# Kernel optimization log

Hardware: AMD Instinct MI355X
Metric: run time of the kernel (lower is better)

## Reference

```python
import jax, jax.numpy as jnp
import numpy as np

B, T, HID = 2, 2048, 2048
NH = 8
D = HID // NH  # head_dim = 256 (expand_ratio=1 so input_dim == hidden_size)
EPS_RMS = 1e-8   # RMSNorm inside BitLinear
EPS_LN = 1e-5    # layernorm_eps for g_norm


def _rms(x, w, eps):
    # weighted RMSNorm over last dim
    return x * jax.lax.rsqrt(jnp.mean(x * x, axis=-1, keepdims=True) + eps) * w


def _act_quant(x):
    # per-token 8-bit fake quant with straight-through estimator
    s = 127.0 / jnp.clip(jnp.max(jnp.abs(x), axis=-1, keepdims=True), 1e-5)
    q = jnp.clip(jnp.round(x * s), -128, 127) / s
    return x + jax.lax.stop_gradient(q - x)


def _weight_quant(w):
    # ternary weight quantization (BitNet b1.58) with STE
    s = 1.0 / jnp.clip(jnp.mean(jnp.abs(w)), 1e-5)
    q = jnp.clip(jnp.round(w * s), -1, 1) / s
    return w + jax.lax.stop_gradient(q - w)


def _bitlinear(x, w, norm_w):
    # FusedBitLinear: RMSNorm -> activation quant -> ternary-weight linear
    xq = _act_quant(_rms(x, norm_w, EPS_RMS))
    return jnp.einsum('btk,ok->bto', xq, _weight_quant(w))


def setup_inputs() -> dict:
    key = jax.random.key(0)
    ks = jax.random.split(key, 5)
    std = 2 ** (-2.5) * np.sqrt(2.0 / (HID + HID))  # xavier_uniform-ish std with gain 2^-2.5
    return {
        'hidden_states': jax.random.normal(ks[0], (B, T, HID), dtype=jnp.float32),
        'w_i': jax.random.normal(ks[1], (HID, HID), dtype=jnp.float32) * std,
        'w_f': jax.random.normal(ks[2], (HID, HID), dtype=jnp.float32) * std,
        'w_g': jax.random.normal(ks[3], (HID, HID), dtype=jnp.float32) * std,
        'w_o': jax.random.normal(ks[4], (HID, HID), dtype=jnp.float32) * std,
        'n_i': jnp.ones((HID,), jnp.float32),
        'n_f': jnp.ones((HID,), jnp.float32),
        'n_g': jnp.ones((HID,), jnp.float32),
        'n_o': jnp.ones((HID,), jnp.float32),
        'gn_w': jnp.ones((HID,), jnp.float32),
    }


def reference(hidden_states, w_i, w_f, w_g, w_o, n_i, n_f, n_g, n_o, gn_w):
    hs = hidden_states
    i = _bitlinear(hs, w_i, n_i)                      # [B,T,HID]
    f = jax.nn.sigmoid(_bitlinear(hs, w_f, n_f))      # forget gate
    # swiglu(i, 1 - f) = silu(i) * (1 - f)
    i = i * jax.nn.sigmoid(i) * (1.0 - f)

    # b l (h d) -> t b h d for scan
    def to_tbhd(x):
        return x.reshape(B, T, NH, D).transpose(1, 0, 2, 3)

    i_t, f_t = to_tbhd(i), to_tbhd(f)

    def step(h, ft_it):
        ft, it = ft_it
        h = ft * h + it
        return h, h

    h0 = jnp.zeros((B, NH, D), dtype=i.dtype)
    _, o = jax.lax.scan(step, h0, (f_t, i_t))         # [T,B,NH,D]
    o = o.transpose(1, 0, 2, 3).reshape(B, T, HID)     # b l (h d)

    # g_norm(g_proj(hs), o): rmsnorm(g) * o * sigmoid(o)
    g = _bitlinear(hs, w_g, n_g)
    o = _rms(g, gn_w, EPS_LN) * o * jax.nn.sigmoid(o)
    return _bitlinear(o, w_o, n_o)
```

## Files before the change

### kernel.cpp

```cpp
#include <hip/hip_runtime.h>
#include <math.h>

#define HID 2048
#define TOKENS 4096
#define TT 2048
#define NCH 4096
#define NC 32
#define CL 64
#define WELEM 4194304

typedef unsigned short u16;
typedef signed char i8;
typedef int i32x4 __attribute__((ext_vector_type(4)));

__device__ inline float sigm(float x) { return 1.0f / (1.0f + expf(-x)); }
__device__ inline u16 f2bf_rn(float v) {
  unsigned b = __float_as_uint(v);
  unsigned r = b + 0x7FFFu + ((b >> 16) & 1u);
  return (u16)(r >> 16);
}
__device__ inline float bf2f(u16 h) {
  return __uint_as_float((unsigned)h << 16);
}

__device__ inline float wred_sum(float v) {
#pragma unroll
  for (int o = 32; o > 0; o >>= 1) v += __shfl_down(v, o);
  return v;
}
__device__ inline float wred_max(float v) {
#pragma unroll
  for (int o = 32; o > 0; o >>= 1) v = fmaxf(v, __shfl_down(v, o));
  return v;
}
__device__ inline double wred_sumd(double v) {
#pragma unroll
  for (int o = 32; o > 0; o >>= 1) v += __shfl_down(v, o);
  return v;
}

__device__ __forceinline__ void gl_lds16(const void* g, void* l) {
  __builtin_amdgcn_global_load_lds(
      (__attribute__((address_space(1))) void*)(void*)g,
      (__attribute__((address_space(3))) void*)l, 16, 0, 0);
}

__device__ __forceinline__ int pack8(const int* qi) {
  return (qi[0] & 255) | ((qi[1] & 255) << 8) | ((qi[2] & 255) << 16)
       | ((qi[3] & 255) << 24);
}

__global__ __launch_bounds__(256) void absmean_kernel(
    const float* __restrict__ w0, const float* __restrict__ w1,
    const float* __restrict__ w2, const float* __restrict__ w3,
    double* __restrict__ wsum) {
  int widx = blockIdx.x >> 9;
  int blk = blockIdx.x & 511;
  const float* w = widx == 0 ? w0 : widx == 1 ? w1 : widx == 2 ? w2 : w3;
  size_t base = (size_t)blk * 8192;
  double acc = 0.0;
#pragma unroll
  for (int r = 0; r < 8; ++r) {
    float4 v = *(const float4*)&w[base + (size_t)(r * 256 + threadIdx.x) * 4];
    acc += (double)fabsf(v.x) + (double)fabsf(v.y) + (double)fabsf(v.z) +
           (double)fabsf(v.w);
  }
  acc = wred_sumd(acc);
  __shared__ double sh[4];
  int tid = threadIdx.x;
  if ((tid & 63) == 0) sh[tid >> 6] = acc;
  __syncthreads();
  if (tid == 0) atomicAdd(&wsum[widx], (sh[0] + sh[1]) + (sh[2] + sh[3]));
}

__global__ __launch_bounds__(256) void wquant4_kernel(
    const float* __restrict__ w0, const float* __restrict__ w1,
    const float* __restrict__ w2, const float* __restrict__ w3,
    const double* __restrict__ wsum, i8* __restrict__ q0, i8* __restrict__ q1,
    i8* __restrict__ q2, i8* __restrict__ q3) {
  int sel = blockIdx.x >> 11;
  int blk = blockIdx.x & 2047;
  const float* w = sel == 0 ? w0 : sel == 1 ? w1 : sel == 2 ? w2 : w3;
  i8* wq = sel == 0 ? q0 : sel == 1 ? q1 : sel == 2 ? q2 : q3;
  int widx = sel == 0 ? 1 : sel == 1 ? 0 : sel;
  double mean = wsum[widx] * (1.0 / (double)WELEM);
  float s = (float)(1.0 / fmax(mean, 1e-5));
  size_t base = (size_t)blk * 2048 + (size_t)threadIdx.x * 8;
  float4 va = *(const float4*)&w[base];
  float4 vb = *(const float4*)&w[base + 4];
  float vv[8] = {va.x, va.y, va.z, va.w, vb.x, vb.y, vb.z, vb.w};
  int qi[8];
#pragma unroll
  for (int j = 0; j < 8; ++j) {
    float q1v = rintf(vv[j] * s);
    q1v = fminf(fmaxf(q1v, -1.0f), 1.0f);
    qi[j] = (int)q1v;
  }
  *(int2*)&wq[base] = make_int2(pack8(qi), pack8(qi + 4));
}

__global__ __launch_bounds__(256) void rmsquant3_kernel(
    const float* __restrict__ X, const float* __restrict__ nw0,
    const float* __restrict__ nw1, const float* __restrict__ nw2,
    i8* __restrict__ Xq0, i8* __restrict__ Xq1, i8* __restrict__ Xq2,
    float* __restrict__ inv0, float* __restrict__ inv1,
    float* __restrict__ inv2) {
  int tok = blockIdx.x;
  int tid = threadIdx.x;
  const float* xrow = X + (size_t)tok * HID;
  int c0 = tid * 8;
  float x[8];
  *(float4*)&x[0] = *(const float4*)&xrow[c0];
  *(float4*)&x[4] = *(const float4*)&xrow[c0 + 4];
  float ss = 0.0f;
#pragma unroll
  for (int j = 0; j < 8; ++j) ss += x[j] * x[j];
  __shared__ float sh[4];
  float v = wred_sum(ss);
  if ((tid & 63) == 0) sh[tid >> 6] = v;
  __syncthreads();
  float tot = (sh[0] + sh[1]) + (sh[2] + sh[3]);
  float rstd = (float)(1.0 / sqrt((double)(tot * (1.0f / HID)) + 1e-8));
#pragma unroll
  for (int pass = 0; pass < 3; ++pass) {
    const float* nw = pass == 0 ? nw0 : pass == 1 ? nw1 : nw2;
    i8* Xq = pass == 0 ? Xq0 : pass == 1 ? Xq1 : Xq2;
    float* inv_s = pass == 0 ? inv0 : pass == 1 ? inv1 : inv2;
    float y[8];
    float amax = 0.0f;
#pragma unroll
    for (int j = 0; j < 8; ++j) {
      y[j] = x[j] * rstd * nw[c0 + j];
      amax = fmaxf(amax, fabsf(y[j]));
    }
    __syncthreads();
    float vv = wred_max(amax);
    if ((tid & 63) == 0) sh[tid >> 6] = vv;
    __syncthreads();
    float am = fmaxf(fmaxf(fmaxf(sh[0], sh[1]), fmaxf(sh[2], sh[3])), 1e-5f);
    float s = 127.0f / am;
    int qi[8];
#pragma unroll
    for (int j = 0; j < 8; ++j) {
      float qq = rintf(y[j] * s);
      qq = fminf(fmaxf(qq, -128.0f), 127.0f);
      qi[j] = (int)qq;
    }
    *(int2*)&Xq[(size_t)tok * HID + c0] = make_int2(pack8(qi), pack8(qi + 4));
    if (tid == 0) inv_s[tok] = am * (1.0f / 127.0f);
  }
}

template <int NSEG, bool F32OUT>
__global__ __launch_bounds__(512) void gemm8_kernel(
    const i8* __restrict__ A0, const i8* __restrict__ A1,
    const i8* __restrict__ A2, const i8* __restrict__ W0,
    const i8* __restrict__ W1, const i8* __restrict__ W2,
    const float* __restrict__ inv0, const float* __restrict__ inv1,
    const float* __restrict__ inv2, const double* __restrict__ wsum,
    int widx0, int widx1, int widx2, void* __restrict__ O0,
    void* __restrict__ O1, void* __restrict__ O2) {
  const int tid = threadIdx.x;
  const int cpx = gridDim.x >> 3;
  const int lid = blockIdx.x;
  const int swz = (lid & 7) * cpx + (lid >> 3);
  const int seg = NSEG == 1 ? 0 : (swz >> 9);
  const int idx = swz & 511;
  const int n0 = (idx & 15) * 128;
  const int m0 = (idx >> 4) * 128;

  const i8* Aq = seg == 0 ? A0 : seg == 1 ? A1 : A2;
  const i8* Wq = seg == 0 ? W0 : seg == 1 ? W1 : W2;
  const float* inv_s = seg == 0 ? inv0 : seg == 1 ? inv1 : inv2;
  void* Out = seg == 0 ? O0 : seg == 1 ? O1 : O2;
  const int widx = seg == 0 ? widx0 : seg == 1 ? widx1 : widx2;

  __shared__ __align__(16) i8 As[2][16384];
  __shared__ __align__(16) i8 Bs[2][16384];
  float wscale = (float)fmax(wsum[widx] * (1.0 / (double)WELEM), 1e-5);

  const int wave = tid >> 6, lane = tid & 63;
  const int wm = wave >> 2;
  const int wn = wave & 3;
  const int lrow = lane & 15;
  const int ksel = lane >> 4;
  const int rsw = lrow & 7;
  const int srow8 = lane >> 3;
  const int scol = ((lane & 7) ^ srow8) << 4;

  const i8* Ab = Aq + (size_t)m0 * HID;
  const i8* Wb = Wq + (size_t)n0 * HID;

  i32x4 acc[4][2];
#pragma unroll
  for (int i = 0; i < 4; ++i)
#pragma unroll
    for (int j = 0; j < 2; ++j)
#pragma unroll
      for (int r = 0; r < 4; ++r) acc[i][j][r] = 0;

#define STAGE(buf, k0)                                                      \
  {                                                                         \
    _Pragma("unroll") for (int c = 0; c < 2; ++c) {                         \
      int chunk = wave * 2 + c;                                             \
      int row = chunk * 8 + srow8;                                          \
      gl_lds16(&Ab[(size_t)row * HID + (k0) + scol], &As[buf][chunk * 1024]); \
      gl_lds16(&Wb[(size_t)row * HID + (k0) + scol], &Bs[buf][chunk * 1024]); \
    }                                                                       \
  }

  const int NT = HID / 128;
  STAGE(0, 0)
  __syncthreads();
  int cur = 0;
  for (int kt = 0; kt < NT; ++kt) {
    if (kt + 1 < NT) STAGE(cur ^ 1, (kt + 1) * 128)
    i32x4 af[4][2], bfr[2][2];
#pragma unroll
    for (int i = 0; i < 4; ++i) {
      int ra = wm * 64 + i * 16 + lrow;
#pragma unroll
      for (int kk = 0; kk < 2; ++kk) {
        int phys = ((kk << 2) | ksel) ^ rsw;
        af[i][kk] = *(const i32x4*)&As[cur][ra * 128 + phys * 16];
      }
    }
#pragma unroll
    for (int j = 0; j < 2; ++j) {
      int rb = wn * 32 + j * 16 + lrow;
#pragma unroll
      for (int kk = 0; kk < 2; ++kk) {
        int phys = ((kk << 2) | ksel) ^ rsw;
        bfr[j][kk] = *(const i32x4*)&Bs[cur][rb * 128 + phys * 16];
      }
    }
    __builtin_amdgcn_s_setprio(1);
#pragma unroll
    for (int kk = 0; kk < 2; ++kk)
#pragma unroll
      for (int i = 0; i < 4; ++i)
#pragma unroll
        for (int j = 0; j < 2; ++j)
          acc[i][j] = __builtin_amdgcn_mfma_i32_16x16x64_i8(
              af[i][kk], bfr[j][kk], acc[i][j], 0, 0, 0);
    __builtin_amdgcn_s_setprio(0);
    __syncthreads();
    cur ^= 1;
  }
#undef STAGE

#pragma unroll
  for (int i = 0; i < 4; ++i) {
    int rbase = m0 + wm * 64 + i * 16 + (lane >> 4) * 4;
#pragma unroll
    for (int j = 0; j < 2; ++j) {
      int col = n0 + wn * 32 + j * 16 + lrow;
#pragma unroll
      for (int r = 0; r < 4; ++r) {
        int row = rbase + r;
        float v = (float)acc[i][j][r] * inv_s[row] * wscale;
        float rr;
        if (NSEG == 3)
          rr = seg == 0 ? sigm(v) : seg == 1 ? v * sigm(v) : v;
        else
          rr = v;
        size_t oidx = (size_t)row * HID + col;
        if (F32OUT)
          ((float*)Out)[oidx] = rr;
        else
          ((u16*)Out)[oidx] = f2bf_rn(rr);
      }
    }
  }
}

__global__ __launch_bounds__(256) void scan1_kernel(
    const u16* __restrict__ F, u16* __restrict__ IO, float* __restrict__ P,
    float* __restrict__ H) {
  int c = blockIdx.x * 256 + threadIdx.x;
  int q = blockIdx.y;
  size_t base =
      (size_t)(c >> 11) * TT * HID + (c & 2047) + (size_t)q * CL * HID;
  float h = 0.0f, p = 1.0f;
#pragma unroll 4
  for (int t = 0; t < CL; ++t) {
    size_t idx = base + (size_t)t * HID;
    float f = bf2f(F[idx]);
    float iv = bf2f(IO[idx]);
    h = fmaf(f, h, iv - iv * f);
    p *= f;
    IO[idx] = f2bf_rn(h);
  }
  P[q * NCH + c] = p;
  H[q * NCH + c] = h;
}

__global__ __launch_bounds__(256) void scan2_kernel(
    const float* __restrict__ P, const float* __restrict__ H,
    float* __restrict__ Ini) {
  int c = blockIdx.x * 256 + threadIdx.x;
  float carry = 0.0f;
#pragma unroll
  for (int q = 0; q < NC; ++q) {
    float pq = P[q * NCH + c];
    float hq = H[q * NCH + c];
    Ini[q * NCH + c] = carry;
    carry = fmaf(pq, carry, hq);
  }
}

__global__ __launch_bounds__(256) void scan3_kernel(
    const u16* __restrict__ F, const float* __restrict__ Ini,
    u16* __restrict__ IO) {
  int c = blockIdx.x * 256 + threadIdx.x;
  int q = blockIdx.y + 1;
  float h0 = Ini[q * NCH + c];
  if (h0 == 0.0f) return;
  size_t base =
      (size_t)(c >> 11) * TT * HID + (c & 2047) + (size_t)q * CL * HID;
  float p = 1.0f;
#pragma unroll 4
  for (int t = 0; t < CL; ++t) {
    size_t idx = base + (size_t)t * HID;
    p *= bf2f(F[idx]);
    IO[idx] = f2bf_rn(fmaf(p, h0, bf2f(IO[idx])));
  }
}

__global__ __launch_bounds__(256) void combine_quant_kernel(
    const u16* __restrict__ G, const float* __restrict__ gnw,
    const u16* __restrict__ O, const float* __restrict__ nw,
    i8* __restrict__ Xq, float* __restrict__ inv_s) {
  int tok = blockIdx.x;
  int tid = threadIdx.x;
  int c0 = tid * 8;
  const u16* grow = G + (size_t)tok * HID;
  const u16* orow = O + (size_t)tok * HID;
  ushort4 ga = *(const ushort4*)&grow[c0];
  ushort4 gb = *(const ushort4*)&grow[c0 + 4];
  ushort4 oa = *(const ushort4*)&orow[c0];
  ushort4 ob = *(const ushort4*)&orow[c0 + 4];
  float g[8] = {bf2f(ga.x), bf2f(ga.y), bf2f(ga.z), bf2f(ga.w),
                bf2f(gb.x), bf2f(gb.y), bf2f(gb.z), bf2f(gb.w)};
  float o[8] = {bf2f(oa.x), bf2f(oa.y), bf2f(oa.z), bf2f(oa.w),
                bf2f(ob.x), bf2f(ob.y), bf2f(ob.z), bf2f(ob.w)};
  __shared__ float sh[4];
  float ss = 0.0f;
#pragma unroll
  for (int j = 0; j < 8; ++j) ss += g[j] * g[j];
  float v = wred_sum(ss);
  if ((tid & 63) == 0) sh[tid >> 6] = v;
  __syncthreads();
  float tot = (sh[0] + sh[1]) + (sh[2] + sh[3]);
  float rstd_g = (float)(1.0 / sqrt((double)(tot * (1.0f / HID)) + 1e-5));
  float on[8];
  float ss2 = 0.0f;
#pragma unroll
  for (int j = 0; j < 8; ++j) {
    on[j] = g[j] * rstd_g * gnw[c0 + j] * o[j] * sigm(o[j]);
    ss2 += on[j] * on[j];
  }
  __syncthreads();
  v = wred_sum(ss2);
  if ((tid & 63) == 0) sh[tid >> 6] = v;
  __syncthreads();
  float tot2 = (sh[0] + sh[1]) + (sh[2] + sh[3]);
  float rstd_o = (float)(1.0 / sqrt((double)(tot2 * (1.0f / HID)) + 1e-8));
  float y[8];
  float amax = 0.0f;
#pragma unroll
  for (int j = 0; j < 8; ++j) {
    y[j] = on[j] * rstd_o * nw[c0 + j];
    amax = fmaxf(amax, fabsf(y[j]));
  }
  __syncthreads();
  v = wred_max(amax);
  if ((tid & 63) == 0) sh[tid >> 6] = v;
  __syncthreads();
  float am = fmaxf(fmaxf(fmaxf(sh[0], sh[1]), fmaxf(sh[2], sh[3])), 1e-5f);
  float s = 127.0f / am;
  int qi[8];
#pragma unroll
  for (int j = 0; j < 8; ++j) {
    float qq = rintf(y[j] * s);
    qq = fminf(fmaxf(qq, -128.0f), 127.0f);
    qi[j] = (int)qq;
  }
  *(int2*)&Xq[(size_t)tok * HID + c0] = make_int2(pack8(qi), pack8(qi + 4));
  if (tid == 0) inv_s[tok] = am * (1.0f / 127.0f);
}

extern "C" void kernel_launch(void* const* d_in, const int* in_sizes, int n_in,
                              void* d_out, int out_size, void* d_ws,
                              size_t ws_size, hipStream_t stream) {
  const float* hs = (const float*)d_in[0];
  const float* w_i = (const float*)d_in[1];
  const float* w_f = (const float*)d_in[2];
  const float* w_g = (const float*)d_in[3];
  const float* w_o = (const float*)d_in[4];
  const float* n_i = (const float*)d_in[5];
  const float* n_f = (const float*)d_in[6];
  const float* n_g = (const float*)d_in[7];
  const float* n_o = (const float*)d_in[8];
  const float* gn_w = (const float*)d_in[9];
  float* Out = (float*)d_out;

  char* ws = (char*)d_ws;
  i8* WQ0 = (i8*)ws;
  i8* WQ1 = (i8*)(ws + 4194304);
  i8* WQ2 = (i8*)(ws + 8388608);
  i8* WQ3 = (i8*)(ws + 12582912);
  i8* XQ0 = (i8*)(ws + 16777216);
  i8* XQ1 = (i8*)(ws + 25165824);
  i8* XQ2 = (i8*)(ws + 33554432);
  u16* F = (u16*)(ws + 41943040);
  u16* OB = (u16*)(ws + 58720256);
  u16* G = (u16*)(ws + 75497472);
  float* invs0 = (float*)(ws + 92274688);
  float* invs1 = (float*)(ws + 92291072);
  float* invs2 = (float*)(ws + 92307456);
  double* wsum = (double*)(ws + 92323840);
  float* scanP = (float*)(ws + 92324864);
  float* scanH = (float*)(ws + 92849152);

  hipMemsetAsync(wsum, 0, 4 * sizeof(double), stream);
  absmean_kernel<<<2048, 256, 0, stream>>>(w_i, w_f, w_g, w_o, wsum);

  wquant4_kernel<<<8192, 256, 0, stream>>>(w_f, w_i, w_g, w_o, wsum, WQ0, WQ1,
                                           WQ2, WQ3);
  rmsquant3_kernel<<<TOKENS, 256, 0, stream>>>(hs, n_f, n_i, n_g, XQ0, XQ1,
                                               XQ2, invs0, invs1, invs2);

  gemm8_kernel<3, false><<<1536, 512, 0, stream>>>(
      XQ0, XQ1, XQ2, WQ0, WQ1, WQ2, invs0, invs1, invs2, wsum, 1, 0, 2, F, OB,
      G);

  scan1_kernel<<<dim3(NCH / 256, NC), 256, 0, stream>>>(F, OB, scanP, scanH);
  scan2_kernel<<<NCH / 256, 256, 0, stream>>>(scanP, scanH, scanP);
  scan3_kernel<<<dim3(NCH / 256, NC - 1), 256, 0, stream>>>(F, scanP, OB);

  combine_quant_kernel<<<TOKENS, 256, 0, stream>>>(G, gn_w, OB, n_o, XQ0,
                                                   invs0);

  gemm8_kernel<1, true><<<512, 512, 0, stream>>>(
      XQ0, XQ0, XQ0, WQ3, WQ3, WQ3, invs0, invs0, invs0, wsum, 3, 3, 3, Out,
      Out, Out);
}
```

Baseline: 200.9 us.

## Enlarge GEMM tile to 128x256 with BK=64, fuse prep and scan kernels

The int8 GEMM tile grows from 128x128 to 128x256 with a K step of 64 and a new LDS swizzle. This doubles the accumulators per wave and halves the grid, to cut global and LDS traffic per MFMA. The weight-quant and activation-quant kernels are merged into one launch, and scan2/scan3 are fused so each block recomputes its chunk carry serially, trading launches for redundant work. The larger tile raises register pressure and leaves fewer blocks (768 and 256) on the device, which may underfill the CUs.

New measurement: 217.6 us. 1.08x slower.

```diff
diff --git a/kernel.cpp b/kernel.cpp
--- a/kernel.cpp
+++ b/kernel.cpp
@@ -73,39 +73,38 @@
   if (tid == 0) atomicAdd(&wsum[widx], (sh[0] + sh[1]) + (sh[2] + sh[3]));
 }
 
-__global__ __launch_bounds__(256) void wquant4_kernel(
+__global__ __launch_bounds__(256) void prep_kernel(
     const float* __restrict__ w0, const float* __restrict__ w1,
     const float* __restrict__ w2, const float* __restrict__ w3,
     const double* __restrict__ wsum, i8* __restrict__ q0, i8* __restrict__ q1,
-    i8* __restrict__ q2, i8* __restrict__ q3) {
-  int sel = blockIdx.x >> 11;
-  int blk = blockIdx.x & 2047;
-  const float* w = sel == 0 ? w0 : sel == 1 ? w1 : sel == 2 ? w2 : w3;
-  i8* wq = sel == 0 ? q0 : sel == 1 ? q1 : sel == 2 ? q2 : q3;
-  int widx = sel == 0 ? 1 : sel == 1 ? 0 : sel;
-  double mean = wsum[widx] * (1.0 / (double)WELEM);
-  float s = (float)(1.0 / fmax(mean, 1e-5));
-  size_t base = (size_t)blk * 2048 + (size_t)threadIdx.x * 8;
-  float4 va = *(const float4*)&w[base];
-  float4 vb = *(const float4*)&w[base + 4];
-  float vv[8] = {va.x, va.y, va.z, va.w, vb.x, vb.y, vb.z, vb.w};
-  int qi[8];
-#pragma unroll
-  for (int j = 0; j < 8; ++j) {
-    float q1v = rintf(vv[j] * s);
-    q1v = fminf(fmaxf(q1v, -1.0f), 1.0f);
-    qi[j] = (int)q1v;
-  }
-  *(int2*)&wq[base] = make_int2(pack8(qi), pack8(qi + 4));
-}
-
-__global__ __launch_bounds__(256) void rmsquant3_kernel(
-    const float* __restrict__ X, const float* __restrict__ nw0,
-    const float* __restrict__ nw1, const float* __restrict__ nw2,
-    i8* __restrict__ Xq0, i8* __restrict__ Xq1, i8* __restrict__ Xq2,
-    float* __restrict__ inv0, float* __restrict__ inv1,
+    i8* __restrict__ q2, i8* __restrict__ q3, const float* __restrict__ X,
+    const float* __restrict__ nw0, const float* __restrict__ nw1,
+    const float* __restrict__ nw2, i8* __restrict__ Xq0, i8* __restrict__ Xq1,
+    i8* __restrict__ Xq2, float* __restrict__ inv0, float* __restrict__ inv1,
     float* __restrict__ inv2) {
-  int tok = blockIdx.x;
+  if (blockIdx.x < 8192) {
+    int sel = blockIdx.x >> 11;
+    int blk = blockIdx.x & 2047;
+    const float* w = sel == 0 ? w0 : sel == 1 ? w1 : sel == 2 ? w2 : w3;
+    i8* wq = sel == 0 ? q0 : sel == 1 ? q1 : sel == 2 ? q2 : q3;
+    int widx = sel == 0 ? 1 : sel == 1 ? 0 : sel;
+    double mean = wsum[widx] * (1.0 / (double)WELEM);
+    float s = (float)(1.0 / fmax(mean, 1e-5));
+    size_t base = (size_t)blk * 2048 + (size_t)threadIdx.x * 8;
+    float4 va = *(const float4*)&w[base];
+    float4 vb = *(const float4*)&w[base + 4];
+    float vv[8] = {va.x, va.y, va.z, va.w, vb.x, vb.y, vb.z, vb.w};
+    int qi[8];
+#pragma unroll
+    for (int j = 0; j < 8; ++j) {
+      float q1v = rintf(vv[j] * s);
+      q1v = fminf(fmaxf(q1v, -1.0f), 1.0f);
+      qi[j] = (int)q1v;
+    }
+    *(int2*)&wq[base] = make_int2(pack8(qi), pack8(qi + 4));
+    return;
+  }
+  int tok = blockIdx.x - 8192;
   int tid = threadIdx.x;
   const float* xrow = X + (size_t)tok * HID;
   int c0 = tid * 8;
@@ -152,7 +151,7 @@
 }
 
 template <int NSEG, bool F32OUT>
-__global__ __launch_bounds__(512) void gemm8_kernel(
+__global__ __launch_bounds__(512, 4) void gemm8_kernel(
     const i8* __restrict__ A0, const i8* __restrict__ A1,
     const i8* __restrict__ A2, const i8* __restrict__ W0,
     const i8* __restrict__ W1, const i8* __restrict__ W2,
@@ -164,10 +163,10 @@
   const int cpx = gridDim.x >> 3;
   const int lid = blockIdx.x;
   const int swz = (lid & 7) * cpx + (lid >> 3);
-  const int seg = NSEG == 1 ? 0 : (swz >> 9);
-  const int idx = swz & 511;
-  const int n0 = (idx & 15) * 128;
-  const int m0 = (idx >> 4) * 128;
+  const int seg = NSEG == 1 ? 0 : (swz >> 8);
+  const int idx = swz & 255;
+  const int n0 = (idx & 7) * 256;
+  const int m0 = (idx >> 3) * 128;
 
   const i8* Aq = seg == 0 ? A0 : seg == 1 ? A1 : A2;
   const i8* Wq = seg == 0 ? W0 : seg == 1 ? W1 : W2;
@@ -175,7 +174,7 @@
   void* Out = seg == 0 ? O0 : seg == 1 ? O1 : O2;
   const int widx = seg == 0 ? widx0 : seg == 1 ? widx1 : widx2;
 
-  __shared__ __align__(16) i8 As[2][16384];
+  __shared__ __align__(16) i8 As[2][8192];
   __shared__ __align__(16) i8 Bs[2][16384];
   float wscale = (float)fmax(wsum[widx] * (1.0 / (double)WELEM), 1e-5);
 
@@ -184,65 +183,57 @@
   const int wn = wave & 3;
   const int lrow = lane & 15;
   const int ksel = lane >> 4;
-  const int rsw = lrow & 7;
-  const int srow8 = lane >> 3;
-  const int scol = ((lane & 7) ^ srow8) << 4;
+  const int phys = ((ksel ^ ((lrow >> 1) & 3)) << 4);
+  const int srl = lane >> 2;
+  const int sg = (lane >> 3) & 3;
+  const int skoff = ((lane & 3) ^ sg) << 4;
 
   const i8* Ab = Aq + (size_t)m0 * HID;
   const i8* Wb = Wq + (size_t)n0 * HID;
 
-  i32x4 acc[4][2];
+  i32x4 acc[4][4];
 #pragma unroll
   for (int i = 0; i < 4; ++i)
 #pragma unroll
-    for (int j = 0; j < 2; ++j)
+    for (int j = 0; j < 4; ++j)
 #pragma unroll
       for (int r = 0; r < 4; ++r) acc[i][j][r] = 0;
 
-#define STAGE(buf, k0)                                                      \
-  {                                                                         \
-    _Pragma("unroll") for (int c = 0; c < 2; ++c) {                         \
-      int chunk = wave * 2 + c;                                             \
-      int row = chunk * 8 + srow8;                                          \
-      gl_lds16(&Ab[(size_t)row * HID + (k0) + scol], &As[buf][chunk * 1024]); \
-      gl_lds16(&Wb[(size_t)row * HID + (k0) + scol], &Bs[buf][chunk * 1024]); \
-    }                                                                       \
-  }
-
-  const int NT = HID / 128;
+#define STAGE(buf, k0)                                                        \
+  {                                                                           \
+    int rowA = wave * 16 + srl;                                               \
+    gl_lds16(&Ab[(size_t)rowA * HID + (k0) + skoff], &As[buf][wave * 1024]);  \
+    int rowB0 = wave * 32 + srl;                                              \
+    gl_lds16(&Wb[(size_t)rowB0 * HID + (k0) + skoff], &Bs[buf][wave * 2048]); \
+    int rowB1 = wave * 32 + 16 + srl;                                         \
+    gl_lds16(&Wb[(size_t)rowB1 * HID + (k0) + skoff],                         \
+             &Bs[buf][wave * 2048 + 1024]);                                   \
+  }
+
+  const int NT = HID / 64;
   STAGE(0, 0)
   __syncthreads();
   int cur = 0;
   for (int kt = 0; kt < NT; ++kt) {
-    if (kt + 1 < NT) STAGE(cur ^ 1, (kt + 1) * 128)
-    i32x4 af[4][2], bfr[2][2];
+    if (kt + 1 < NT) STAGE(cur ^ 1, (kt + 1) * 64)
+    i32x4 af[4], bfr[4];
 #pragma unroll
     for (int i = 0; i < 4; ++i) {
       int ra = wm * 64 + i * 16 + lrow;
-#pragma unroll
-      for (int kk = 0; kk < 2; ++kk) {
-        int phys = ((kk << 2) | ksel) ^ rsw;
-        af[i][kk] = *(const i32x4*)&As[cur][ra * 128 + phys * 16];
-      }
-    }
-#pragma unroll
-    for (int j = 0; j < 2; ++j) {
-      int rb = wn * 32 + j * 16 + lrow;
-#pragma unroll
-      for (int kk = 0; kk < 2; ++kk) {
-        int phys = ((kk << 2) | ksel) ^ rsw;
-        bfr[j][kk] = *(const i32x4*)&Bs[cur][rb * 128 + phys * 16];
-      }
+      af[i] = *(const i32x4*)&As[cur][ra * 64 + phys];
+    }
+#pragma unroll
+    for (int j = 0; j < 4; ++j) {
+      int rb = wn * 64 + j * 16 + lrow;
+      bfr[j] = *(const i32x4*)&Bs[cur][rb * 64 + phys];
     }
     __builtin_amdgcn_s_setprio(1);
 #pragma unroll
-    for (int kk = 0; kk < 2; ++kk)
-#pragma unroll
-      for (int i = 0; i < 4; ++i)
-#pragma unroll
-        for (int j = 0; j < 2; ++j)
-          acc[i][j] = __builtin_amdgcn_mfma_i32_16x16x64_i8(
-              af[i][kk], bfr[j][kk], acc[i][j], 0, 0, 0);
+    for (int i = 0; i < 4; ++i)
+#pragma unroll
+      for (int j = 0; j < 4; ++j)
+        acc[i][j] = __builtin_amdgcn_mfma_i32_16x16x64_i8(af[i], bfr[j],
+                                                          acc[i][j], 0, 0, 0);
     __builtin_amdgcn_s_setprio(0);
     __syncthreads();
     cur ^= 1;
@@ -253,8 +244,8 @@
   for (int i = 0; i < 4; ++i) {
     int rbase = m0 + wm * 64 + i * 16 + (lane >> 4) * 4;
 #pragma unroll
-    for (int j = 0; j < 2; ++j) {
-      int col = n0 + wn * 32 + j * 16 + lrow;
+    for (int j = 0; j < 4; ++j) {
+      int col = n0 + wn * 64 + j * 16 + lrow;
 #pragma unroll
       for (int r = 0; r < 4; ++r) {
         int row = rbase + r;
@@ -295,27 +286,15 @@
   H[q * NCH + c] = h;
 }
 
-__global__ __launch_bounds__(256) void scan2_kernel(
-    const float* __restrict__ P, const float* __restrict__ H,
-    float* __restrict__ Ini) {
-  int c = blockIdx.x * 256 + threadIdx.x;
-  float carry = 0.0f;
-#pragma unroll
-  for (int q = 0; q < NC; ++q) {
-    float pq = P[q * NCH + c];
-    float hq = H[q * NCH + c];
-    Ini[q * NCH + c] = carry;
-    carry = fmaf(pq, carry, hq);
-  }
-}
-
-__global__ __launch_bounds__(256) void scan3_kernel(
-    const u16* __restrict__ F, const float* __restrict__ Ini,
-    u16* __restrict__ IO) {
+__global__ __launch_bounds__(256) void scan23_kernel(
+    const u16* __restrict__ F, const float* __restrict__ P,
+    const float* __restrict__ H, u16* __restrict__ IO) {
   int c = blockIdx.x * 256 + threadIdx.x;
   int q = blockIdx.y + 1;
-  float h0 = Ini[q * NCH + c];
-  if (h0 == 0.0f) return;
+  float carry = 0.0f;
+  for (int qq = 0; qq < q; ++qq)
+    carry = fmaf(P[qq * NCH + c], carry, H[qq * NCH + c]);
+  if (carry == 0.0f) return;
   size_t base =
       (size_t)(c >> 11) * TT * HID + (c & 2047) + (size_t)q * CL * HID;
   float p = 1.0f;
@@ -323,7 +302,7 @@
   for (int t = 0; t < CL; ++t) {
     size_t idx = base + (size_t)t * HID;
     p *= bf2f(F[idx]);
-    IO[idx] = f2bf_rn(fmaf(p, h0, bf2f(IO[idx])));
+    IO[idx] = f2bf_rn(fmaf(p, carry, bf2f(IO[idx])));
   }
 }
 
@@ -426,23 +405,22 @@
   hipMemsetAsync(wsum, 0, 4 * sizeof(double), stream);
   absmean_kernel<<<2048, 256, 0, stream>>>(w_i, w_f, w_g, w_o, wsum);
 
-  wquant4_kernel<<<8192, 256, 0, stream>>>(w_f, w_i, w_g, w_o, wsum, WQ0, WQ1,
-                                           WQ2, WQ3);
-  rmsquant3_kernel<<<TOKENS, 256, 0, stream>>>(hs, n_f, n_i, n_g, XQ0, XQ1,
-                                               XQ2, invs0, invs1, invs2);
-
-  gemm8_kernel<3, false><<<1536, 512, 0, stream>>>(
+  prep_kernel<<<12288, 256, 0, stream>>>(w_f, w_i, w_g, w_o, wsum, WQ0, WQ1,
+                                         WQ2, WQ3, hs, n_f, n_i, n_g, XQ0,
+                                         XQ1, XQ2, invs0, invs1, invs2);
+
+  gemm8_kernel<3, false><<<768, 512, 0, stream>>>(
       XQ0, XQ1, XQ2, WQ0, WQ1, WQ2, invs0, invs1, invs2, wsum, 1, 0, 2, F, OB,
       G);
 
   scan1_kernel<<<dim3(NCH / 256, NC), 256, 0, stream>>>(F, OB, scanP, scanH);
-  scan2_kernel<<<NCH / 256, 256, 0, stream>>>(scanP, scanH, scanP);
-  scan3_kernel<<<dim3(NCH / 256, NC - 1), 256, 0, stream>>>(F, scanP, OB);
+  scan23_kernel<<<dim3(NCH / 256, NC - 1), 256, 0, stream>>>(F, scanP, scanH,
+                                                             OB);
 
   combine_quant_kernel<<<TOKENS, 256, 0, stream>>>(G, gn_w, OB, n_o, XQ0,
                                                    invs0);
 
-  gemm8_kernel<1, true><<<512, 512, 0, stream>>>(
+  gemm8_kernel<1, true><<<256, 512, 0, stream>>>(
       XQ0, XQ0, XQ0, WQ3, WQ3, WQ3, invs0, invs0, invs0, wsum, 3, 3, 3, Out,
       Out, Out);
 }
```
